# Optimization experiments

Measured on AMD Instinct MI355X. Metric: run time of the kernel, lower is better.

The kernel has to match this reference:

```python
import jax, jax.numpy as jnp
import numpy as np

B, N, M = 4, 2048, 2048
DIM = 1024
HEADS = 16
DIM_HEAD = 64
INNER = HEADS * DIM_HEAD
SCALE = 8.0


def layer_norm(x, g, eps=1e-5):
    mean = jnp.mean(x, axis=-1, keepdims=True)
    var = jnp.mean((x - mean) ** 2, axis=-1, keepdims=True)
    return (x - mean) * jax.lax.rsqrt(var + eps) * g


def l2norm(t, eps=1e-12):
    n = jnp.maximum(jnp.linalg.norm(t, axis=-1, keepdims=True), eps)
    return t / n


def setup_inputs() -> dict:
    key = jax.random.key(0)
    ks = jax.random.split(key, 8)
    x = jax.random.normal(ks[0], (B, N, DIM), dtype=jnp.float32)
    context = jax.random.normal(ks[1], (B, M, DIM), dtype=jnp.float32)
    # parameters
    g_norm = jnp.ones((DIM,), dtype=jnp.float32)
    null_kv = jax.random.normal(ks[2], (2, DIM_HEAD), dtype=jnp.float32)
    Wq = jax.random.normal(ks[3], (DIM, INNER), dtype=jnp.float32) / np.sqrt(DIM)
    Wkv = jax.random.normal(ks[4], (DIM, 2 * INNER), dtype=jnp.float32) / np.sqrt(DIM)
    q_scale = jnp.ones((DIM_HEAD,), dtype=jnp.float32)
    k_scale = jnp.ones((DIM_HEAD,), dtype=jnp.float32)
    Wout = jax.random.normal(ks[5], (INNER, DIM), dtype=jnp.float32) / np.sqrt(INNER)
    g_out = jnp.ones((DIM,), dtype=jnp.float32)
    return {"x": x, "context": context, "g_norm": g_norm, "null_kv": null_kv,
            "Wq": Wq, "Wkv": Wkv, "q_scale": q_scale, "k_scale": k_scale,
            "Wout": Wout, "g_out": g_out}


def reference(x, context, g_norm, null_kv, Wq, Wkv, q_scale, k_scale, Wout, g_out):
    b = x.shape[0]
    xn = layer_norm(x, g_norm)            # [b, n, dim]
    ctx = context                          # norm_context=False -> Identity
    q = xn @ Wq                            # [b, n, inner]
    kv = ctx @ Wkv                         # [b, m, 2*inner]
    k, v = jnp.split(kv, 2, axis=-1)
    split_heads = lambda t: t.reshape(b, t.shape[1], HEADS, DIM_HEAD).transpose(0, 2, 1, 3)
    q, k, v = map(split_heads, (q, k, v))  # [b, h, n|m, d]
    # null kv token prepended along the key/value sequence dim
    nk = jnp.broadcast_to(null_kv[0], (b, HEADS, 1, DIM_HEAD))
    nv = jnp.broadcast_to(null_kv[1], (b, HEADS, 1, DIM_HEAD))
    k = jnp.concatenate([nk, k], axis=2)   # [b, h, m+1, d]
    v = jnp.concatenate([nv, v], axis=2)
    # QK-norm with learned per-dim scales
    q = l2norm(q) * q_scale
    k = l2norm(k) * k_scale
    sim = jnp.einsum('bhid,bhjd->bhij', q, k) * SCALE
    attn = jax.nn.softmax(sim.astype(jnp.float32), axis=-1).astype(sim.dtype)
    out = jnp.einsum('bhij,bhjd->bhid', attn, v)
    out = out.transpose(0, 2, 1, 3).reshape(b, -1, INNER)  # [b, n, inner]
    out = out @ Wout
    return layer_norm(out, g_out)
```

## Files before the change

kernel.cpp:

```cpp
#include <hip/hip_runtime.h>

#define BATCH 4
#define NSEQ 2048
#define MSEQ 2048
#define DIM 1024
#define HEADS 16
#define DHEAD 64
#define INNER 1024
#define KVLEN 2049
#define KVPAD 2176

typedef unsigned short u16;
typedef unsigned int u32;
typedef __bf16 bf16x8 __attribute__((ext_vector_type(8)));
typedef float f32x4 __attribute__((ext_vector_type(4)));

__device__ inline u16 f2bf(float f) {
  u32 u = __builtin_bit_cast(u32, f);
  u = (u + 0x7fffu + ((u >> 16) & 1u)) >> 16;
  return (u16)u;
}
__device__ inline float bf2f(u16 x) {
  return __builtin_bit_cast(float, (u32)x << 16);
}
__device__ inline u32 pk_bf16(float lo, float hi) {
  u32 r;
  asm("v_cvt_pk_bf16_f32 %0, %1, %2" : "=v"(r) : "v"(lo), "v"(hi));
  return r;
}

__device__ __forceinline__ void gld_lds16(const void* g, void* l) {
  __builtin_amdgcn_global_load_lds(
      (const __attribute__((address_space(1))) void*)g,
      (__attribute__((address_space(3))) void*)l, 16, 0, 0);
}

template <bool OUT_BF16>
__global__ __launch_bounds__(256) void ln_kernel(const float* __restrict__ x,
                                                 const float* __restrict__ g,
                                                 void* __restrict__ out) {
  const int row = blockIdx.x;
  const int t = threadIdx.x;
  const float4 v = ((const float4*)(x + (size_t)row * 1024))[t];
  float sum = v.x + v.y + v.z + v.w;
  float sq = v.x * v.x + v.y * v.y + v.z * v.z + v.w * v.w;
  for (int m = 1; m < 64; m <<= 1) {
    sum += __shfl_xor(sum, m, 64);
    sq += __shfl_xor(sq, m, 64);
  }
  __shared__ float red[8];
  const int w = t >> 6, l = t & 63;
  if (l == 0) { red[w] = sum; red[4 + w] = sq; }
  __syncthreads();
  sum = red[0] + red[1] + red[2] + red[3];
  sq = red[4] + red[5] + red[6] + red[7];
  const float mean = sum * (1.0f / 1024.0f);
  const float var = sq * (1.0f / 1024.0f) - mean * mean;
  const float rstd = rsqrtf(var + 1e-5f);
  const float4 gv = ((const float4*)g)[t];
  float o0 = (v.x - mean) * rstd * gv.x;
  float o1 = (v.y - mean) * rstd * gv.y;
  float o2 = (v.z - mean) * rstd * gv.z;
  float o3 = (v.w - mean) * rstd * gv.w;
  if (OUT_BF16) {
    ushort4 ov;
    ov.x = f2bf(o0); ov.y = f2bf(o1); ov.z = f2bf(o2); ov.w = f2bf(o3);
    ((ushort4*)((u16*)out + (size_t)row * 1024))[t] = ov;
  } else {
    float4 ov;
    ov.x = o0; ov.y = o1; ov.z = o2; ov.w = o3;
    ((float4*)((float*)out + (size_t)row * 1024))[t] = ov;
  }
}

__global__ __launch_bounds__(256) void cast_bf16(const float* __restrict__ in,
                                                 u16* __restrict__ out, int n4) {
  int i = blockIdx.x * 256 + threadIdx.x;
  if (i < n4) {
    float4 v = ((const float4*)in)[i];
    ushort4 o;
    o.x = f2bf(v.x); o.y = f2bf(v.y); o.z = f2bf(v.z); o.w = f2bf(v.w);
    ((ushort4*)out)[i] = o;
  }
}

__global__ __launch_bounds__(256) void transpose_cast(const float* __restrict__ W,
                                                      u16* __restrict__ WT, int K, int N) {
  __shared__ float tile[32][33];
  const int tx = threadIdx.x & 31, ty = threadIdx.x >> 5;
  const int k0 = blockIdx.y * 32, n0 = blockIdx.x * 32;
  for (int r = ty; r < 32; r += 8) tile[r][tx] = W[(size_t)(k0 + r) * N + n0 + tx];
  __syncthreads();
  for (int r = ty; r < 32; r += 8) WT[(size_t)(n0 + r) * K + k0 + tx] = f2bf(tile[tx][r]);
}

template <int MODE>
__global__ __launch_bounds__(256) void gemm_bt(const u16* __restrict__ A,
                                               const u16* __restrict__ Bt,
                                               void* __restrict__ Cv,
                                               int M, int N, int K,
                                               const float* __restrict__ scale,
                                               u16* __restrict__ aux) {
  __shared__ __align__(16) u16 As[128 * 32];
  __shared__ __align__(16) u16 Bs[128 * 32];
  const int t = threadIdx.x;
  const int w = t >> 6, l = t & 63, l15 = l & 15, lq = l >> 4;
  const int m0 = blockIdx.y * 128, n0 = blockIdx.x * 128;
  const int wm = (w >> 1) * 64, wn = (w & 1) * 64;
  const int lr = l >> 2;
  const int lo = (l & 3) * 8;
  f32x4 acc[4][4] = {};
  for (int k0 = 0; k0 < K; k0 += 32) {
#pragma unroll
    for (int it = 0; it < 2; it++) {
      const int row = (w * 2 + it) * 16 + lr;
      gld_lds16(&A[(size_t)(m0 + row) * K + k0 + lo], &As[row * 32 + lo]);
      gld_lds16(&Bt[(size_t)(n0 + row) * K + k0 + lo], &Bs[row * 32 + lo]);
    }
    __syncthreads();
    bf16x8 af[4], bfr[4];
#pragma unroll
    for (int i = 0; i < 4; i++) af[i] = *(bf16x8*)&As[(wm + i * 16 + l15) * 32 + lq * 8];
#pragma unroll
    for (int j = 0; j < 4; j++) bfr[j] = *(bf16x8*)&Bs[(wn + j * 16 + l15) * 32 + lq * 8];
#pragma unroll
    for (int i = 0; i < 4; i++)
#pragma unroll
      for (int j = 0; j < 4; j++)
        acc[i][j] = __builtin_amdgcn_mfma_f32_16x16x32_bf16(af[i], bfr[j], acc[i][j], 0, 0, 0);
    __syncthreads();
  }

  if (MODE <= 1) {
#pragma unroll
    for (int i = 0; i < 4; i++)
#pragma unroll
      for (int j = 0; j < 4; j++)
#pragma unroll
        for (int r = 0; r < 4; r++) {
          const size_t off =
              (size_t)(m0 + wm + i * 16 + lq * 4 + r) * N + n0 + wn + j * 16 + l15;
          if (MODE == 1) ((u16*)Cv)[off] = f2bf(acc[i][j][r]);
          else ((float*)Cv)[off] = acc[i][j][r];
        }
    return;
  }

  const int head = (n0 + wn) >> 6;
  if (MODE == 3 && head >= 16) {
#pragma unroll
    for (int i = 0; i < 4; i++)
#pragma unroll
      for (int j = 0; j < 4; j++)
#pragma unroll
        for (int r = 0; r < 4; r++) {
          const int row = m0 + wm + i * 16 + lq * 4 + r;
          aux[(size_t)row * 1024 + (head - 16) * 64 + j * 16 + l15] = f2bf(acc[i][j][r]);
        }
    return;
  }
  float sc[4];
#pragma unroll
  for (int j = 0; j < 4; j++) sc[j] = scale[j * 16 + l15];
  const float mul = (MODE == 2) ? 8.0f : 1.0f;
  u16* outp = (u16*)Cv;
#pragma unroll
  for (int i = 0; i < 4; i++)
#pragma unroll
    for (int r = 0; r < 4; r++) {
      float ss = 0.f;
#pragma unroll
      for (int j = 0; j < 4; j++) ss = fmaf(acc[i][j][r], acc[i][j][r], ss);
#pragma unroll
      for (int m = 1; m < 16; m <<= 1) ss += __shfl_xor(ss, m, 64);
      const float inv = mul / fmaxf(sqrtf(ss), 1e-12f);
      const int row = m0 + wm + i * 16 + lq * 4 + r;
      const int b = row >> 11, n = row & 2047;
      const size_t base = (MODE == 2)
          ? (((size_t)b * 16 + head) * 2048 + n) * 64
          : (((size_t)b * 16 + head) * (size_t)KVPAD + n + 1) * 64;
#pragma unroll
      for (int j = 0; j < 4; j++)
        outp[base + j * 16 + l15] = f2bf(acc[i][j][r] * inv * sc[j]);
    }
}

__global__ __launch_bounds__(256) void v_post(const u16* __restrict__ vg,
                                              u16* __restrict__ vt) {
  __shared__ u16 tile[64][68];
  const int bh = blockIdx.y, mt = blockIdx.x;
  const int tx = threadIdx.x & 63, ty = threadIdx.x >> 6;
  const int b = bh >> 4, h = bh & 15;
  const int m0 = mt * 64;
  for (int r = ty; r < 64; r += 4)
    tile[tx][r] = vg[(size_t)(b * 2048 + m0 + r) * 1024 + h * 64 + tx];
  __syncthreads();
  const int abs_ = 1 + m0 + tx;
  const int slot = (abs_ & ~127) | ((abs_ & 15) << 3) | ((abs_ >> 4) & 7);
  for (int d = ty; d < 64; d += 4)
    vt[((size_t)bh * 64 + d) * KVPAD + slot] = tile[d][tx];
}

__global__ __launch_bounds__(64) void null_tail(const float* __restrict__ null_kv,
                                                const float* __restrict__ k_scale,
                                                u16* __restrict__ kn, u16* __restrict__ vt) {
  const int bh = blockIdx.x, d = threadIdx.x;
  float nk = null_kv[d];
  float nv = null_kv[64 + d];
  float ss = nk * nk;
  for (int m = 1; m < 64; m <<= 1) ss += __shfl_xor(ss, m, 64);
  float inv = 1.0f / fmaxf(sqrtf(ss), 1e-12f);
  kn[((size_t)bh * KVPAD) * 64 + d] = f2bf(nk * inv * k_scale[d]);
  vt[((size_t)bh * 64 + d) * KVPAD] = f2bf(nv);
  for (int m = KVLEN; m < KVPAD; m++) kn[((size_t)bh * KVPAD + m) * 64 + d] = 0;
  u16* vrow = vt + ((size_t)bh * 64 + d) * KVPAD;
  for (int m = KVLEN; m < KVPAD; m++) vrow[m] = 0;
}

__global__ __launch_bounds__(256, 4) void attn_kernel(const u16* __restrict__ qn,
                                                      const u16* __restrict__ kn,
                                                      const u16* __restrict__ vt,
                                                      u16* __restrict__ aout) {
  __shared__ __align__(16) u16 KPs[128 * 72];
  __shared__ __align__(16) u16 Vs[64 * 136];
  const int qt = blockIdx.x, bh = blockIdx.y;
  const int b = bh >> 4, h = bh & 15;
  const int t = threadIdx.x, w = t >> 6, l = t & 63, l15 = l & 15, lq = l >> 4;

  bf16x8 aqf[2];
  {
    const u16* qrow = qn + ((size_t)bh * 2048 + qt * 64 + w * 16 + l15) * 64 + lq * 8;
    aqf[0] = *(const bf16x8*)(qrow);
    aqf[1] = *(const bf16x8*)(qrow + 32);
  }

  const int krow = t >> 3, kko = (t & 7) * 8;
  const u16* kgp = kn + (size_t)bh * KVPAD * 64 + krow * 64 + kko;
  u16* klp = (u16*)&KPs[krow * 72 + kko];
  const int vd = t >> 4, voff = (t & 15) * 8;
  const u16* vgp = vt + ((size_t)bh * 64 + vd) * KVPAD + voff;
  u16* vlp = (u16*)&Vs[vd * 136 + voff];

  f32x4 O[4] = {};
  float lsum[4] = {0.f, 0.f, 0.f, 0.f};
  const float LOG2E = 1.44269504f;
  const float MBIAS = -8.0f * 1.44269504f;

  for (int kt = 0; kt < 17; kt++) {
#pragma unroll
    for (int i = 0; i < 4; i++)
      *(uint4*)(klp + i * 2304) = *(const uint4*)(kgp + kt * 8192 + i * 2048);
#pragma unroll
    for (int i = 0; i < 4; i++)
      *(uint4*)(vlp + i * 2176) = *(const uint4*)(vgp + kt * 128 + (size_t)i * 16 * KVPAD);
    __syncthreads();

    f32x4 S[8] = {};
    __builtin_amdgcn_s_setprio(1);
#pragma unroll
    for (int ks = 0; ks < 2; ks++)
#pragma unroll
      for (int j = 0; j < 8; j++) {
        bf16x8 bk = *(bf16x8*)&KPs[(j * 16 + l15) * 72 + ks * 32 + lq * 8];
        S[j] = __builtin_amdgcn_mfma_f32_16x16x32_bf16(aqf[ks], bk, S[j], 0, 0, 0);
      }
    __builtin_amdgcn_s_setprio(0);
    __syncthreads();

    const bool last = (kt == 16);
#pragma unroll
    for (int r = 0; r < 4; r++) {
      float pe[8];
#pragma unroll
      for (int j = 0; j < 8; j++) {
        float p = __builtin_amdgcn_exp2f(fmaf(S[j][r], LOG2E, MBIAS));
        if (last && ((j << 4) | l15) != 0) p = 0.f;
        lsum[r] += p;
        pe[j] = p;
      }
      uint4 pw;
      pw.x = pk_bf16(pe[0], pe[1]);
      pw.y = pk_bf16(pe[2], pe[3]);
      pw.z = pk_bf16(pe[4], pe[5]);
      pw.w = pk_bf16(pe[6], pe[7]);
      *(uint4*)&KPs[(w * 16 + lq * 4 + r) * 136 + l15 * 8] = pw;
    }

    __builtin_amdgcn_s_setprio(1);
#pragma unroll
    for (int ks = 0; ks < 4; ks++) {
      bf16x8 ap = *(bf16x8*)&KPs[(w * 16 + l15) * 136 + ks * 32 + lq * 8];
#pragma unroll
      for (int nt = 0; nt < 4; nt++) {
        bf16x8 bv = *(bf16x8*)&Vs[(nt * 16 + l15) * 136 + ks * 32 + lq * 8];
        O[nt] = __builtin_amdgcn_mfma_f32_16x16x32_bf16(ap, bv, O[nt], 0, 0, 0);
      }
    }
    __builtin_amdgcn_s_setprio(0);
    __syncthreads();
  }

#pragma unroll
  for (int r = 0; r < 4; r++)
#pragma unroll
    for (int m = 1; m < 16; m <<= 1) lsum[r] += __shfl_xor(lsum[r], m, 64);
#pragma unroll
  for (int nt = 0; nt < 4; nt++)
#pragma unroll
    for (int r = 0; r < 4; r++) {
      int row = qt * 64 + w * 16 + lq * 4 + r;
      int col = h * 64 + nt * 16 + l15;
      float val = O[nt][r] / lsum[r];
      aout[((size_t)b * 2048 + row) * 1024 + col] = f2bf(val);
    }
}

extern "C" void kernel_launch(void* const* d_in, const int* in_sizes, int n_in,
                              void* d_out, int out_size, void* d_ws, size_t ws_size,
                              hipStream_t stream) {
  const float* x = (const float*)d_in[0];
  const float* context = (const float*)d_in[1];
  const float* g_norm = (const float*)d_in[2];
  const float* null_kv = (const float*)d_in[3];
  const float* Wq = (const float*)d_in[4];
  const float* Wkv = (const float*)d_in[5];
  const float* q_scale = (const float*)d_in[6];
  const float* k_scale = (const float*)d_in[7];
  const float* Wout = (const float*)d_in[8];
  const float* g_out = (const float*)d_in[9];
  float* out = (float*)d_out;

  char* ws = (char*)d_ws;
  u16* xn = (u16*)(ws);
  u16* ctxb = (u16*)(ws + 16777216);
  u16* wqT = (u16*)(ws + 33554432);
  u16* wkvT = (u16*)(ws + 35651584);
  u16* woutT = (u16*)(ws + 39845888);
  u16* qnb = (u16*)(ws + 41943040);
  u16* knb = (u16*)(ws + 58720256);
  u16* vtb = (u16*)(ws + 76546048);
  u16* vg = (u16*)(ws + 94371840);
  float* outg = (float*)(ws + 111149056);
  u16* attn_out = vg;

  ln_kernel<true><<<8192, 256, 0, stream>>>(x, g_norm, xn);
  cast_bf16<<<8192, 256, 0, stream>>>(context, ctxb, 2097152);
  transpose_cast<<<dim3(32, 32), 256, 0, stream>>>(Wq, wqT, 1024, 1024);
  transpose_cast<<<dim3(64, 32), 256, 0, stream>>>(Wkv, wkvT, 1024, 2048);
  transpose_cast<<<dim3(32, 32), 256, 0, stream>>>(Wout, woutT, 1024, 1024);
  gemm_bt<2><<<dim3(8, 64), 256, 0, stream>>>(xn, wqT, qnb, 8192, 1024, 1024, q_scale, nullptr);
  gemm_bt<3><<<dim3(16, 64), 256, 0, stream>>>(ctxb, wkvT, knb, 8192, 2048, 1024, k_scale, vg);
  v_post<<<dim3(32, 64), 256, 0, stream>>>(vg, vtb);
  null_tail<<<64, 64, 0, stream>>>(null_kv, k_scale, knb, vtb);
  attn_kernel<<<dim3(32, 64), 256, 0, stream>>>(qnb, knb, vtb, attn_out);
  gemm_bt<0><<<dim3(8, 64), 256, 0, stream>>>(attn_out, woutT, outg, 8192, 1024, 1024, nullptr, nullptr);
  ln_kernel<false><<<8192, 256, 0, stream>>>(outg, g_out, out);
}
```

Baseline: 426.6 us.

## Read K/V MFMA fragments directly from global and drop LDS staging in attention

The attention kernel no longer stages each K and V tile into shared memory behind block-wide barriers. Each wave now loads its MFMA B-operand fragments straight from global memory, and only the softmax probabilities go through a smaller per-wave LDS buffer, so all __syncthreads in the loop are removed. The cost is that all four waves fetch the same K/V data separately, which raises L2 traffic and leaves global load latency more exposed. The null_tail kernel is also spread over 256 threads, so the padding-zeroing loops run in four interleaved segments.

```diff
diff --git a/kernel.cpp b/kernel.cpp
--- a/kernel.cpp
+++ b/kernel.cpp
@@ -201,28 +201,30 @@
     vt[((size_t)bh * 64 + d) * KVPAD + slot] = tile[d][tx];
 }
 
-__global__ __launch_bounds__(64) void null_tail(const float* __restrict__ null_kv,
-                                                const float* __restrict__ k_scale,
-                                                u16* __restrict__ kn, u16* __restrict__ vt) {
-  const int bh = blockIdx.x, d = threadIdx.x;
-  float nk = null_kv[d];
-  float nv = null_kv[64 + d];
-  float ss = nk * nk;
-  for (int m = 1; m < 64; m <<= 1) ss += __shfl_xor(ss, m, 64);
-  float inv = 1.0f / fmaxf(sqrtf(ss), 1e-12f);
-  kn[((size_t)bh * KVPAD) * 64 + d] = f2bf(nk * inv * k_scale[d]);
-  vt[((size_t)bh * 64 + d) * KVPAD] = f2bf(nv);
-  for (int m = KVLEN; m < KVPAD; m++) kn[((size_t)bh * KVPAD + m) * 64 + d] = 0;
+__global__ __launch_bounds__(256) void null_tail(const float* __restrict__ null_kv,
+                                                 const float* __restrict__ k_scale,
+                                                 u16* __restrict__ kn, u16* __restrict__ vt) {
+  const int bh = blockIdx.x, t = threadIdx.x;
+  const int d = t & 63, seg = t >> 6;
+  if (seg == 0) {
+    float nk = null_kv[d];
+    float nv = null_kv[64 + d];
+    float ss = nk * nk;
+    for (int m = 1; m < 64; m <<= 1) ss += __shfl_xor(ss, m, 64);
+    float inv = 1.0f / fmaxf(sqrtf(ss), 1e-12f);
+    kn[((size_t)bh * KVPAD) * 64 + d] = f2bf(nk * inv * k_scale[d]);
+    vt[((size_t)bh * 64 + d) * KVPAD] = f2bf(nv);
+  }
+  for (int m = KVLEN + seg; m < KVPAD; m += 4) kn[((size_t)bh * KVPAD + m) * 64 + d] = 0;
   u16* vrow = vt + ((size_t)bh * 64 + d) * KVPAD;
-  for (int m = KVLEN; m < KVPAD; m++) vrow[m] = 0;
+  for (int m = KVLEN + seg; m < KVPAD; m += 4) vrow[m] = 0;
 }
 
 __global__ __launch_bounds__(256, 4) void attn_kernel(const u16* __restrict__ qn,
                                                       const u16* __restrict__ kn,
                                                       const u16* __restrict__ vt,
                                                       u16* __restrict__ aout) {
-  __shared__ __align__(16) u16 KPs[128 * 72];
-  __shared__ __align__(16) u16 Vs[64 * 136];
+  __shared__ __align__(16) u16 Ps[64 * 136];
   const int qt = blockIdx.x, bh = blockIdx.y;
   const int b = bh >> 4, h = bh & 15;
   const int t = threadIdx.x, w = t >> 6, l = t & 63, l15 = l & 15, lq = l >> 4;
@@ -234,12 +236,8 @@
     aqf[1] = *(const bf16x8*)(qrow + 32);
   }
 
-  const int krow = t >> 3, kko = (t & 7) * 8;
-  const u16* kgp = kn + (size_t)bh * KVPAD * 64 + krow * 64 + kko;
-  u16* klp = (u16*)&KPs[krow * 72 + kko];
-  const int vd = t >> 4, voff = (t & 15) * 8;
-  const u16* vgp = vt + ((size_t)bh * 64 + vd) * KVPAD + voff;
-  u16* vlp = (u16*)&Vs[vd * 136 + voff];
+  const u16* kptr = kn + (size_t)bh * KVPAD * 64 + l15 * 64 + lq * 8;
+  const u16* vptr = vt + ((size_t)bh * 64 + l15) * KVPAD + lq * 8;
 
   f32x4 O[4] = {};
   float lsum[4] = {0.f, 0.f, 0.f, 0.f};
@@ -247,25 +245,16 @@
   const float MBIAS = -8.0f * 1.44269504f;
 
   for (int kt = 0; kt < 17; kt++) {
-#pragma unroll
-    for (int i = 0; i < 4; i++)
-      *(uint4*)(klp + i * 2304) = *(const uint4*)(kgp + kt * 8192 + i * 2048);
-#pragma unroll
-    for (int i = 0; i < 4; i++)
-      *(uint4*)(vlp + i * 2176) = *(const uint4*)(vgp + kt * 128 + (size_t)i * 16 * KVPAD);
-    __syncthreads();
-
     f32x4 S[8] = {};
     __builtin_amdgcn_s_setprio(1);
 #pragma unroll
     for (int ks = 0; ks < 2; ks++)
 #pragma unroll
       for (int j = 0; j < 8; j++) {
-        bf16x8 bk = *(bf16x8*)&KPs[(j * 16 + l15) * 72 + ks * 32 + lq * 8];
+        bf16x8 bk = *(const bf16x8*)(kptr + kt * 8192 + j * 1024 + ks * 32);
         S[j] = __builtin_amdgcn_mfma_f32_16x16x32_bf16(aqf[ks], bk, S[j], 0, 0, 0);
       }
     __builtin_amdgcn_s_setprio(0);
-    __syncthreads();
 
     const bool last = (kt == 16);
 #pragma unroll
@@ -283,21 +272,20 @@
       pw.y = pk_bf16(pe[2], pe[3]);
       pw.z = pk_bf16(pe[4], pe[5]);
       pw.w = pk_bf16(pe[6], pe[7]);
-      *(uint4*)&KPs[(w * 16 + lq * 4 + r) * 136 + l15 * 8] = pw;
+      *(uint4*)&Ps[(w * 16 + lq * 4 + r) * 136 + l15 * 8] = pw;
     }
 
     __builtin_amdgcn_s_setprio(1);
 #pragma unroll
     for (int ks = 0; ks < 4; ks++) {
-      bf16x8 ap = *(bf16x8*)&KPs[(w * 16 + l15) * 136 + ks * 32 + lq * 8];
+      bf16x8 ap = *(bf16x8*)&Ps[(w * 16 + l15) * 136 + ks * 32 + lq * 8];
 #pragma unroll
       for (int nt = 0; nt < 4; nt++) {
-        bf16x8 bv = *(bf16x8*)&Vs[(nt * 16 + l15) * 136 + ks * 32 + lq * 8];
+        bf16x8 bv = *(const bf16x8*)(vptr + (size_t)nt * 16 * KVPAD + kt * 128 + ks * 32);
         O[nt] = __builtin_amdgcn_mfma_f32_16x16x32_bf16(ap, bv, O[nt], 0, 0, 0);
       }
     }
     __builtin_amdgcn_s_setprio(0);
-    __syncthreads();
   }
 
 #pragma unroll
@@ -351,7 +339,7 @@
   gemm_bt<2><<<dim3(8, 64), 256, 0, stream>>>(xn, wqT, qnb, 8192, 1024, 1024, q_scale, nullptr);
   gemm_bt<3><<<dim3(16, 64), 256, 0, stream>>>(ctxb, wkvT, knb, 8192, 2048, 1024, k_scale, vg);
   v_post<<<dim3(32, 64), 256, 0, stream>>>(vg, vtb);
-  null_tail<<<64, 64, 0, stream>>>(null_kv, k_scale, knb, vtb);
+  null_tail<<<64, 256, 0, stream>>>(null_kv, k_scale, knb, vtb);
   attn_kernel<<<dim3(32, 64), 256, 0, stream>>>(qnb, knb, vtb, attn_out);
   gemm_bt<0><<<dim3(8, 64), 256, 0, stream>>>(attn_out, woutT, outg, 8192, 1024, 1024, nullptr, nullptr);
   ln_kernel<false><<<8192, 256, 0, stream>>>(outg, g_out, out);
```

Result: slower. 773.7 us (+81.4%).
